# Kernel optimization log

Measured on AMD Instinct MI355X. Metric: run time of the kernel, lower is better.

Reference implementation:

```python
import jax, jax.numpy as jnp
import numpy as np

B, S, D, P = 8, 2048, 512, 64  # batch, seq, num_embed_hidden, num_attention_project


def setup_inputs() -> dict:
    key = jax.random.key(0)
    ks = jax.random.split(key, 9)
    sd = 1.0 / np.sqrt(D)
    sp = 1.0 / np.sqrt(P)
    return {
        "query": jax.random.normal(ks[0], (B, S, D), dtype=jnp.float32),
        "attention_mask": jnp.ones((B, S), dtype=jnp.float32),
        "Wq": jax.random.uniform(ks[1], (D, P), jnp.float32, -sd, sd),
        "bq": jax.random.uniform(ks[2], (P,), jnp.float32, -sd, sd),
        "Wk": jax.random.uniform(ks[3], (D, P), jnp.float32, -sd, sd),
        "bk": jax.random.uniform(ks[4], (P,), jnp.float32, -sd, sd),
        "Wv": jax.random.uniform(ks[5], (D, P), jnp.float32, -sd, sd),
        "bv": jax.random.uniform(ks[6], (P,), jnp.float32, -sd, sd),
        "Wo": jax.random.uniform(ks[7], (P, D), jnp.float32, -sp, sp),
        "bo": jax.random.uniform(ks[8], (D,), jnp.float32, -sp, sp),
    }


def reference(query, attention_mask, Wq, bq, Wk, bk, Wv, bv, Wo, bo):
    q = jnp.einsum("bsd,dp->bsp", query, Wq) + bq  # [B,S,P]
    k = jnp.einsum("bsd,dp->bsp", query, Wk) + bk
    v = jnp.einsum("bsd,dp->bsp", query, Wv) + bv
    scores = jnp.einsum("bsp,btp->bst", q, k) / jnp.sqrt(jnp.float32(P))  # [B,S,S]
    # Faithful to original: mask broadcast over last axis via unsqueeze(-1) -> masks rows
    scores = scores + (1.0 - attention_mask[:, :, None]) * -10000.0
    weights = jax.nn.softmax(scores, axis=-1)
    weighted = jnp.einsum("bst,btp->bsp", weights, v)
    return jnp.einsum("bsp,pd->bsd", weighted, Wo) + bo
```

## Files before the change

### kernel.cpp

```cpp
#include <hip/hip_runtime.h>
#include <hip/hip_bf16.h>
#include <math.h>

constexpr int B = 8;
constexpr int S = 2048;
constexpr int D = 512;
constexpr int P = 64;
constexpr float SCALE = 0.125f;

typedef short bf16x8 __attribute__((ext_vector_type(8)));
typedef float f32x4 __attribute__((ext_vector_type(4)));
typedef unsigned int u32;

__device__ __forceinline__ unsigned short f2bf(float x) {
  __hip_bfloat16 h = __float2bfloat16(x);
  return __builtin_bit_cast(unsigned short, h);
}
__device__ __forceinline__ float bf2f(unsigned short u) {
  unsigned int v = (unsigned int)u << 16;
  return __builtin_bit_cast(float, v);
}

__device__ __forceinline__ void ld_g2lds16(const unsigned short* g,
                                           unsigned short* l) {
  __builtin_amdgcn_global_load_lds(
      (const __attribute__((address_space(1))) u32*)g,
      (__attribute__((address_space(3))) u32*)l, 16, 0, 0);
}

__global__ __launch_bounds__(256) void prep_w(
    const float* __restrict__ Wq, const float* __restrict__ Wk,
    const float* __restrict__ Wv, const float* __restrict__ Wo,
    unsigned short* __restrict__ WcatT, unsigned short* __restrict__ WoT) {
  const int i = blockIdx.x * 256 + threadIdx.x;
  if (i < 192 * 512) {
    const int n = i >> 9, k = i & 511;
    const float* W = (n < 64) ? Wq : (n < 128) ? Wk : Wv;
    WcatT[i] = f2bf(W[k * 64 + (n & 63)]);
  }
  if (i < 512 * 64) {
    WoT[i] = f2bf(Wo[(i & 63) * 512 + (i >> 6)]);
  }
}

__global__ __launch_bounds__(256, 2) void qkv_mfma(
    const float* __restrict__ query, const unsigned short* __restrict__ WcatT,
    const float* __restrict__ bq, const float* __restrict__ bk,
    const float* __restrict__ bv, unsigned short* __restrict__ q_bf,
    unsigned short* __restrict__ k_bf, unsigned short* __restrict__ vT_bf) {
  __shared__ __align__(16) unsigned short Aq[32 * 512];
  __shared__ __align__(16) unsigned short Bb[2][192 * 64];

  const int tid = threadIdx.x;
  const int w = tid >> 6;
  const int l = tid & 63;
  const int l15 = l & 15;
  const int l4 = l >> 4;
  const int s0 = blockIdx.x * 32;
  const int rg = w & 1;
  const int ch = w >> 1;

  const float* qsrc = query + (size_t)s0 * D;
  for (int step = 0; step < 8; ++step) {
    const int row = step * 4 + w;
    const float* pf = qsrc + row * D + l * 8;
    const float4 x = *(const float4*)pf;
    const float4 y = *(const float4*)(pf + 4);
    bf16x8 u;
    u[0] = (short)f2bf(x.x); u[1] = (short)f2bf(x.y);
    u[2] = (short)f2bf(x.z); u[3] = (short)f2bf(x.w);
    u[4] = (short)f2bf(y.x); u[5] = (short)f2bf(y.y);
    u[6] = (short)f2bf(y.z); u[7] = (short)f2bf(y.w);
    *(bf16x8*)&Aq[row * 512 + ((l ^ (row & 7)) << 3)] = u;
  }

#pragma unroll
  for (int c = 0; c < 6; ++c) {
    const int n = c * 32 + w * 8 + (l >> 3);
    const unsigned short* gp =
        WcatT + (size_t)n * 512 + (((l & 7) ^ (l >> 3)) << 3);
    ld_g2lds16(gp, &Bb[0][(c * 256 + w * 64) * 8]);
  }
  __syncthreads();

  f32x4 acc[6];
#pragma unroll
  for (int nt = 0; nt < 6; ++nt) acc[nt] = (f32x4){0.f, 0.f, 0.f, 0.f};

  for (int kc = 0; kc < 8; ++kc) {
    if (kc < 7) {
#pragma unroll
      for (int c = 0; c < 6; ++c) {
        const int n = c * 32 + w * 8 + (l >> 3);
        const unsigned short* gp = WcatT + (size_t)n * 512 + (kc + 1) * 64 +
                                   (((l & 7) ^ (l >> 3)) << 3);
        ld_g2lds16(gp, &Bb[(kc + 1) & 1][(c * 256 + w * 64) * 8]);
      }
    }
    const unsigned short* Bcur = &Bb[kc & 1][0];
#pragma unroll
    for (int kk = 0; kk < 2; ++kk) {
      const int row = rg * 16 + l15;
      const int aslot = (kc * 8 + kk * 4 + l4) ^ (row & 7);
      const bf16x8 af = *(const bf16x8*)&Aq[row * 512 + (aslot << 3)];
      bf16x8 bfr[6];
#pragma unroll
      for (int nt = 0; nt < 6; ++nt) {
        const int n = ch * 96 + nt * 16 + l15;
        const int slot = (kk * 4 + l4) ^ (n & 7);
        bfr[nt] = *(const bf16x8*)&Bcur[n * 64 + (slot << 3)];
      }
#pragma unroll
      for (int nt = 0; nt < 6; ++nt)
        acc[nt] = __builtin_amdgcn_mfma_f32_16x16x32_bf16(af, bfr[nt], acc[nt],
                                                          0, 0, 0);
    }
    __syncthreads();
  }

  const int batch = s0 >> 11;
  const int sloc = s0 & 2047;
#pragma unroll
  for (int nt = 0; nt < 6; ++nt) {
    const int col = ch * 96 + nt * 16 + l15;
    const int mat = col >> 6;
    const int p = col & 63;
    const float bb = ((mat == 0) ? bq : (mat == 1) ? bk : bv)[p];
#pragma unroll
    for (int r = 0; r < 4; ++r) {
      const int row = rg * 16 + l4 * 4 + r;
      const float vl = acc[nt][r] + bb;
      if (mat == 0)
        q_bf[(size_t)(s0 + row) * P + p] = f2bf(vl * SCALE);
      else if (mat == 1)
        k_bf[(size_t)(s0 + row) * P + p] = f2bf(vl);
      else
        vT_bf[((size_t)batch * P + p) * S + sloc + row] = f2bf(vl);
    }
  }
}

__global__ __launch_bounds__(512, 2) void attn_fused(
    const unsigned short* __restrict__ q_bf,
    const unsigned short* __restrict__ k_bf,
    const unsigned short* __restrict__ vT_bf,
    const unsigned short* __restrict__ WoT, const float* __restrict__ bo,
    float* __restrict__ out) {
  __shared__ __align__(16) unsigned short kb[2][4][64 * 64];
  __shared__ __align__(16) unsigned short vb[2][4][64 * 64];
  __shared__ __align__(16) unsigned short e_s[8][16 * 64];
  __shared__ float l_s[8][32];

  const int tid = threadIdx.x;
  const int w = tid >> 6;
  const int lane = tid & 63;
  const int l15 = lane & 15;
  const int l4 = lane >> 4;
  const int qg = w & 1;
  const int th = w >> 1;

  const int blk = blockIdx.x;
  const int b = blk & 7;
  const int s0 = (blk >> 3) * 64;

  const unsigned short* qb = q_bf + ((size_t)b * S + s0) * P;
  const unsigned short* kbg = k_bf + (size_t)b * S * P;
  const unsigned short* vtg = vT_bf + (size_t)b * P * S;

  bf16x8 aq[2][2];
#pragma unroll
  for (int st = 0; st < 2; ++st)
#pragma unroll
    for (int h = 0; h < 2; ++h)
      aq[st][h] = *(const bf16x8*)(qb + (size_t)(qg * 32 + st * 16 + l15) * P +
                                   h * 32 + l4 * 8);

  f32x4 acc[2][4];
#pragma unroll
  for (int st = 0; st < 2; ++st)
#pragma unroll
    for (int pc = 0; pc < 4; ++pc) acc[st][pc] = (f32x4){0.f, 0.f, 0.f, 0.f};
  float lpart[2][4] = {{0.f, 0.f, 0.f, 0.f}, {0.f, 0.f, 0.f, 0.f}};

  const int jrow = (lane >> 3);
  const int jch = lane & 7;
  {
    const int t0 = th * 512;
#pragma unroll
    for (int j = 0; j < 8; ++j) {
      if (qg == 0) {
        const unsigned short* gp =
            kbg + ((size_t)t0 + j * 8 + jrow) * P + jch * 8;
        ld_g2lds16(gp, &kb[0][th][j * 512]);
      } else {
        const unsigned short* gp =
            vtg + ((size_t)(j * 8 + jrow)) * S + t0 + jch * 8;
        ld_g2lds16(gp, &vb[0][th][j * 512]);
      }
    }
  }
  __syncthreads();

  for (int win = 0; win < 8; ++win) {
    if (win < 7) {
      const int t0n = th * 512 + (win + 1) * 64;
      const int nb = (win + 1) & 1;
#pragma unroll
      for (int j = 0; j < 8; ++j) {
        if (qg == 0) {
          const unsigned short* gp =
              kbg + ((size_t)t0n + j * 8 + jrow) * P + jch * 8;
          ld_g2lds16(gp, &kb[nb][th][j * 512]);
        } else {
          const unsigned short* gp =
              vtg + ((size_t)(j * 8 + jrow)) * S + t0n + jch * 8;
          ld_g2lds16(gp, &vb[nb][th][j * 512]);
        }
      }
    }

    const unsigned short* kt = &kb[win & 1][th][0];
    const unsigned short* vt = &vb[win & 1][th][0];

    bf16x8 bkf[4][2], bvf[4][2];
#pragma unroll
    for (int nt = 0; nt < 4; ++nt)
#pragma unroll
      for (int h = 0; h < 2; ++h)
        bkf[nt][h] =
            *(const bf16x8*)&kt[(nt * 16 + l15) * 64 + h * 32 + l4 * 8];
#pragma unroll
    for (int pc = 0; pc < 4; ++pc)
#pragma unroll
      for (int kk = 0; kk < 2; ++kk)
        bvf[pc][kk] =
            *(const bf16x8*)&vt[(pc * 16 + l15) * 64 + kk * 32 + l4 * 8];

#pragma unroll
    for (int st = 0; st < 2; ++st) {
      f32x4 sc[4];
#pragma unroll
      for (int nt = 0; nt < 4; ++nt) {
        f32x4 c = (f32x4){0.f, 0.f, 0.f, 0.f};
        c = __builtin_amdgcn_mfma_f32_16x16x32_bf16(aq[st][0], bkf[nt][0], c,
                                                    0, 0, 0);
        sc[nt] = __builtin_amdgcn_mfma_f32_16x16x32_bf16(aq[st][1], bkf[nt][1],
                                                         c, 0, 0, 0);
      }
#pragma unroll
      for (int nt = 0; nt < 4; ++nt) {
        const int ch = nt * 2 + (l15 >> 3);
#pragma unroll
        for (int r = 0; r < 4; ++r) {
          const int rr = l4 * 4 + r;
          const unsigned short eu = f2bf(__expf(sc[nt][r]));
          lpart[st][r] += bf2f(eu);
          e_s[w][rr * 64 + ((ch ^ (rr & 7)) << 3) + (l15 & 7)] = eu;
        }
      }
      bf16x8 ae[2];
#pragma unroll
      for (int kk = 0; kk < 2; ++kk)
        ae[kk] = *(const bf16x8*)&e_s[w][l15 * 64 +
                                         (((kk * 4 + l4) ^ (l15 & 7)) << 3)];
#pragma unroll
      for (int pc = 0; pc < 4; ++pc) {
        acc[st][pc] = __builtin_amdgcn_mfma_f32_16x16x32_bf16(
            ae[0], bvf[pc][0], acc[st][pc], 0, 0, 0);
        acc[st][pc] = __builtin_amdgcn_mfma_f32_16x16x32_bf16(
            ae[1], bvf[pc][1], acc[st][pc], 0, 0, 0);
      }
    }
    __syncthreads();
  }

#pragma unroll
  for (int st = 0; st < 2; ++st) {
#pragma unroll
    for (int r = 0; r < 4; ++r) {
      float v = lpart[st][r];
      v += __shfl_xor(v, 1, 64);
      v += __shfl_xor(v, 2, 64);
      v += __shfl_xor(v, 4, 64);
      v += __shfl_xor(v, 8, 64);
      if (l15 == 0) l_s[w][st * 16 + l4 * 4 + r] = v;
    }
  }

  float* pacc = (float*)&kb[0][0][0];
  if (th > 0) {
#pragma unroll
    for (int st = 0; st < 2; ++st)
#pragma unroll
      for (int pc = 0; pc < 4; ++pc)
#pragma unroll
        for (int r = 0; r < 4; ++r)
          pacc[((size_t)(qg * 3 + th - 1) * 32 + st * 16 + l4 * 4 + r) * 64 +
               pc * 16 + l15] = acc[st][pc][r];
  }
  __syncthreads();

  unsigned short* wnorm = &e_s[0][0];
  if (th == 0) {
#pragma unroll
    for (int st = 0; st < 2; ++st) {
      float rl[4];
#pragma unroll
      for (int r = 0; r < 4; ++r) {
        const int row = st * 16 + l4 * 4 + r;
        rl[r] = 1.f / (l_s[qg][row] + l_s[2 + qg][row] + l_s[4 + qg][row] +
                       l_s[6 + qg][row]);
      }
#pragma unroll
      for (int pc = 0; pc < 4; ++pc)
#pragma unroll
        for (int r = 0; r < 4; ++r) {
          float s = acc[st][pc][r];
#pragma unroll
          for (int j = 0; j < 3; ++j)
            s += pacc[((size_t)(qg * 3 + j) * 32 + st * 16 + l4 * 4 + r) * 64 +
                      pc * 16 + l15];
          wnorm[(qg * 32 + st * 16 + l4 * 4 + r) * 64 + pc * 16 + l15] =
              f2bf(s * rl[r]);
        }
    }
  }
  __syncthreads();

  const int sub = w & 3;
  const int chalf = w >> 2;
  const int qgs = sub >> 1;
  const int lrow = (sub & 1) * 16 + l15;
  const bf16x8 a0 = *(const bf16x8*)&wnorm[(qgs * 32 + lrow) * 64 + l4 * 8];
  const bf16x8 a1 =
      *(const bf16x8*)&wnorm[(qgs * 32 + lrow) * 64 + 32 + l4 * 8];
  const size_t orow0 = (size_t)b * S + s0 + sub * 16;
#pragma unroll
  for (int ct = 0; ct < 16; ++ct) {
    const int col = chalf * 256 + ct * 16 + l15;
    const bf16x8 b0 = *(const bf16x8*)(WoT + (size_t)col * 64 + l4 * 8);
    const bf16x8 b1 = *(const bf16x8*)(WoT + (size_t)col * 64 + 32 + l4 * 8);
    f32x4 c = (f32x4){0.f, 0.f, 0.f, 0.f};
    c = __builtin_amdgcn_mfma_f32_16x16x32_bf16(a0, b0, c, 0, 0, 0);
    c = __builtin_amdgcn_mfma_f32_16x16x32_bf16(a1, b1, c, 0, 0, 0);
    const float bb = bo[col];
#pragma unroll
    for (int r = 0; r < 4; ++r)
      out[(orow0 + l4 * 4 + r) * D + col] = c[r] + bb;
  }
}

extern "C" void kernel_launch(void* const* d_in, const int* in_sizes, int n_in,
                              void* d_out, int out_size, void* d_ws,
                              size_t ws_size, hipStream_t stream) {
  const float* query = (const float*)d_in[0];
  const float* Wq = (const float*)d_in[2];
  const float* bq = (const float*)d_in[3];
  const float* Wk = (const float*)d_in[4];
  const float* bk = (const float*)d_in[5];
  const float* Wv = (const float*)d_in[6];
  const float* bv = (const float*)d_in[7];
  const float* Wo = (const float*)d_in[8];
  const float* bo = (const float*)d_in[9];
  float* out = (float*)d_out;

  const size_t n_rows = (size_t)B * S;
  const size_t proj = n_rows * P;
  unsigned short* qbf = (unsigned short*)d_ws;
  unsigned short* kbf = qbf + proj;
  unsigned short* vtbf = kbf + proj;
  unsigned short* WcatT = vtbf + proj;
  unsigned short* WoT = WcatT + 192 * 512;

  prep_w<<<384, 256, 0, stream>>>(Wq, Wk, Wv, Wo, WcatT, WoT);
  qkv_mfma<<<512, 256, 0, stream>>>(query, WcatT, bq, bk, bv, qbf, kbf, vtbf);
  attn_fused<<<256, 512, 0, stream>>>(qbf, kbf, vtbf, WoT, bo, out);
}
```

Baseline: 140.2 us.

## Store Q/K/V and weights in MFMA fragment layout, drop LDS staging

Intermediate Q, K, V and the weight matrices are now written in a pre-swizzled MFMA fragment order, so each lane loads its operand with one contiguous 16-byte global read. The async global-to-LDS double buffering and per-window block barriers in the attention kernel are removed, and the QKV kernel now uses 16-row tiles with more blocks and a higher occupancy hint. The aim is to cut LDS traffic and synchronisation, relying on L2 and cache for K/V reuse. The risk is that repeated global reads across waves lose the sharing the LDS staging gave and expose load latency without explicit prefetch.

```diff
diff --git a/kernel.cpp b/kernel.cpp
--- a/kernel.cpp
+++ b/kernel.cpp
@@ -21,47 +21,48 @@
   return __builtin_bit_cast(float, v);
 }
 
-__device__ __forceinline__ void ld_g2lds16(const unsigned short* g,
-                                           unsigned short* l) {
-  __builtin_amdgcn_global_load_lds(
-      (const __attribute__((address_space(1))) u32*)g,
-      (__attribute__((address_space(3))) u32*)l, 16, 0, 0);
-}
 
 __global__ __launch_bounds__(256) void prep_w(
     const float* __restrict__ Wq, const float* __restrict__ Wk,
     const float* __restrict__ Wv, const float* __restrict__ Wo,
-    unsigned short* __restrict__ WcatT, unsigned short* __restrict__ WoT) {
+    unsigned short* __restrict__ Bfrag, unsigned short* __restrict__ Wofrag) {
   const int i = blockIdx.x * 256 + threadIdx.x;
   if (i < 192 * 512) {
-    const int n = i >> 9, k = i & 511;
+    const int d = i / 192;
+    const int n = i - d * 192;
     const float* W = (n < 64) ? Wq : (n < 128) ? Wk : Wv;
-    WcatT[i] = f2bf(W[k * 64 + (n & 63)]);
-  }
-  if (i < 512 * 64) {
-    WoT[i] = f2bf(Wo[(i & 63) * 512 + (i >> 6)]);
-  }
-}
-
-__global__ __launch_bounds__(256, 2) void qkv_mfma(
-    const float* __restrict__ query, const unsigned short* __restrict__ WcatT,
+    const float val = W[d * 64 + (n & 63)];
+    const int nt = n >> 4, l15 = n & 15;
+    const int k16 = d >> 5, l4 = (d >> 3) & 3, j = d & 7;
+    Bfrag[(((nt * 16 + k16) * 4 + l4) * 16 + l15) * 8 + j] = f2bf(val);
+  }
+  if (i < 64 * 512) {
+    const int k = i >> 9;
+    const int n = i & 511;
+    const float val = Wo[k * 512 + n];
+    const int ct = n >> 4, l15 = n & 15;
+    const int h = k >> 5, l4 = (k >> 3) & 3, j = k & 7;
+    Wofrag[(((ct * 2 + h) * 4 + l4) * 16 + l15) * 8 + j] = f2bf(val);
+  }
+}
+
+__global__ __launch_bounds__(256, 4) void qkv_mfma(
+    const float* __restrict__ query, const unsigned short* __restrict__ Bfrag,
     const float* __restrict__ bq, const float* __restrict__ bk,
-    const float* __restrict__ bv, unsigned short* __restrict__ q_bf,
-    unsigned short* __restrict__ k_bf, unsigned short* __restrict__ vT_bf) {
-  __shared__ __align__(16) unsigned short Aq[32 * 512];
-  __shared__ __align__(16) unsigned short Bb[2][192 * 64];
+    const float* __restrict__ bv, unsigned short* __restrict__ qfrag,
+    unsigned short* __restrict__ kfrag, unsigned short* __restrict__ vfrag) {
+  __shared__ __align__(16) unsigned short Aq[16 * 512];
 
   const int tid = threadIdx.x;
   const int w = tid >> 6;
   const int l = tid & 63;
   const int l15 = l & 15;
   const int l4 = l >> 4;
-  const int s0 = blockIdx.x * 32;
-  const int rg = w & 1;
-  const int ch = w >> 1;
+  const int s0 = blockIdx.x * 16;
 
   const float* qsrc = query + (size_t)s0 * D;
-  for (int step = 0; step < 8; ++step) {
+#pragma unroll
+  for (int step = 0; step < 4; ++step) {
     const int row = step * 4 + w;
     const float* pf = qsrc + row * D + l * 8;
     const float4 x = *(const float4*)pf;
@@ -73,82 +74,62 @@
     u[6] = (short)f2bf(y.z); u[7] = (short)f2bf(y.w);
     *(bf16x8*)&Aq[row * 512 + ((l ^ (row & 7)) << 3)] = u;
   }
-
-#pragma unroll
-  for (int c = 0; c < 6; ++c) {
-    const int n = c * 32 + w * 8 + (l >> 3);
-    const unsigned short* gp =
-        WcatT + (size_t)n * 512 + (((l & 7) ^ (l >> 3)) << 3);
-    ld_g2lds16(gp, &Bb[0][(c * 256 + w * 64) * 8]);
-  }
   __syncthreads();
 
-  f32x4 acc[6];
-#pragma unroll
-  for (int nt = 0; nt < 6; ++nt) acc[nt] = (f32x4){0.f, 0.f, 0.f, 0.f};
-
-  for (int kc = 0; kc < 8; ++kc) {
-    if (kc < 7) {
-#pragma unroll
-      for (int c = 0; c < 6; ++c) {
-        const int n = c * 32 + w * 8 + (l >> 3);
-        const unsigned short* gp = WcatT + (size_t)n * 512 + (kc + 1) * 64 +
-                                   (((l & 7) ^ (l >> 3)) << 3);
-        ld_g2lds16(gp, &Bb[(kc + 1) & 1][(c * 256 + w * 64) * 8]);
-      }
-    }
-    const unsigned short* Bcur = &Bb[kc & 1][0];
-#pragma unroll
-    for (int kk = 0; kk < 2; ++kk) {
-      const int row = rg * 16 + l15;
-      const int aslot = (kc * 8 + kk * 4 + l4) ^ (row & 7);
-      const bf16x8 af = *(const bf16x8*)&Aq[row * 512 + (aslot << 3)];
-      bf16x8 bfr[6];
-#pragma unroll
-      for (int nt = 0; nt < 6; ++nt) {
-        const int n = ch * 96 + nt * 16 + l15;
-        const int slot = (kk * 4 + l4) ^ (n & 7);
-        bfr[nt] = *(const bf16x8*)&Bcur[n * 64 + (slot << 3)];
-      }
-#pragma unroll
-      for (int nt = 0; nt < 6; ++nt)
-        acc[nt] = __builtin_amdgcn_mfma_f32_16x16x32_bf16(af, bfr[nt], acc[nt],
-                                                          0, 0, 0);
-    }
-    __syncthreads();
-  }
-
-  const int batch = s0 >> 11;
-  const int sloc = s0 & 2047;
-#pragma unroll
-  for (int nt = 0; nt < 6; ++nt) {
-    const int col = ch * 96 + nt * 16 + l15;
+  f32x4 acc[3];
+#pragma unroll
+  for (int nt = 0; nt < 3; ++nt) acc[nt] = (f32x4){0.f, 0.f, 0.f, 0.f};
+
+#pragma unroll
+  for (int k16 = 0; k16 < 16; ++k16) {
+    const int aslot = (k16 * 4 + l4) ^ (l15 & 7);
+    const bf16x8 af = *(const bf16x8*)&Aq[l15 * 512 + (aslot << 3)];
+#pragma unroll
+    for (int nt = 0; nt < 3; ++nt) {
+      const int ntg = w * 3 + nt;
+      const bf16x8 bf =
+          *(const bf16x8*)(Bfrag + ((size_t)(ntg * 16 + k16) * 64 + l) * 8);
+      acc[nt] = __builtin_amdgcn_mfma_f32_16x16x32_bf16(af, bf, acc[nt], 0, 0,
+                                                        0);
+    }
+  }
+
+  const int b = s0 >> 11;
+  const size_t bbase = (size_t)b * (S * P);
+#pragma unroll
+  for (int nt = 0; nt < 3; ++nt) {
+    const int col = w * 48 + nt * 16 + l15;
     const int mat = col >> 6;
     const int p = col & 63;
     const float bb = ((mat == 0) ? bq : (mat == 1) ? bk : bv)[p];
 #pragma unroll
     for (int r = 0; r < 4; ++r) {
-      const int row = rg * 16 + l4 * 4 + r;
+      const int s = s0 + l4 * 4 + r;
+      const int t = s & 2047;
       const float vl = acc[nt][r] + bb;
-      if (mat == 0)
-        q_bf[(size_t)(s0 + row) * P + p] = f2bf(vl * SCALE);
-      else if (mat == 1)
-        k_bf[(size_t)(s0 + row) * P + p] = f2bf(vl);
-      else
-        vT_bf[((size_t)batch * P + p) * S + sloc + row] = f2bf(vl);
-    }
-  }
-}
-
-__global__ __launch_bounds__(512, 2) void attn_fused(
-    const unsigned short* __restrict__ q_bf,
-    const unsigned short* __restrict__ k_bf,
-    const unsigned short* __restrict__ vT_bf,
-    const unsigned short* __restrict__ WoT, const float* __restrict__ bo,
+      if (mat == 2) {
+        const int tb = t >> 5, chv = (t >> 3) & 3, jv = t & 7;
+        const int pcv = p >> 4, rowv = p & 15;
+        vfrag[bbase + (((size_t)(tb * 4 + pcv) * 4 + chv) * 16 + rowv) * 8 +
+              jv] = f2bf(vl);
+      } else {
+        const int tile = t >> 4, rowin = t & 15;
+        const int h = p >> 5, chp = (p >> 3) & 3, j = p & 7;
+        unsigned short* dst = (mat == 0) ? qfrag : kfrag;
+        dst[bbase + (((size_t)(tile * 2 + h) * 4 + chp) * 16 + rowin) * 8 +
+            j] = f2bf(mat == 0 ? vl * SCALE : vl);
+      }
+    }
+  }
+}
+
+__global__ __launch_bounds__(512, 4) void attn_fused(
+    const unsigned short* __restrict__ qfrag,
+    const unsigned short* __restrict__ kfrag,
+    const unsigned short* __restrict__ vfrag,
+    const unsigned short* __restrict__ Wofrag, const float* __restrict__ bo,
     float* __restrict__ out) {
-  __shared__ __align__(16) unsigned short kb[2][4][64 * 64];
-  __shared__ __align__(16) unsigned short vb[2][4][64 * 64];
-  __shared__ __align__(16) unsigned short e_s[8][16 * 64];
+  __shared__ __align__(16) unsigned char smem[57344];
   __shared__ float l_s[8][32];
 
   const int tid = threadIdx.x;
@@ -163,17 +144,23 @@
   const int b = blk & 7;
   const int s0 = (blk >> 3) * 64;
 
-  const unsigned short* qb = q_bf + ((size_t)b * S + s0) * P;
-  const unsigned short* kbg = k_bf + (size_t)b * S * P;
-  const unsigned short* vtg = vT_bf + (size_t)b * P * S;
+  const size_t bbase = (size_t)b * (S * P);
+  const unsigned short* qf = qfrag + bbase;
+  const unsigned short* kf = kfrag + bbase;
+  const unsigned short* vf = vfrag + bbase;
+
+  unsigned short* e_s = (unsigned short*)smem + w * 2048;
 
   bf16x8 aq[2][2];
 #pragma unroll
   for (int st = 0; st < 2; ++st)
 #pragma unroll
     for (int h = 0; h < 2; ++h)
-      aq[st][h] = *(const bf16x8*)(qb + (size_t)(qg * 32 + st * 16 + l15) * P +
-                                   h * 32 + l4 * 8);
+      aq[st][h] = *(const bf16x8*)(qf +
+                                   ((size_t)(((s0 >> 4) + qg * 2 + st) * 2 + h) *
+                                        64 +
+                                    lane) *
+                                       8);
 
   f32x4 acc[2][4];
 #pragma unroll
@@ -182,100 +169,74 @@
     for (int pc = 0; pc < 4; ++pc) acc[st][pc] = (f32x4){0.f, 0.f, 0.f, 0.f};
   float lpart[2][4] = {{0.f, 0.f, 0.f, 0.f}, {0.f, 0.f, 0.f, 0.f}};
 
-  const int jrow = (lane >> 3);
-  const int jch = lane & 7;
-  {
-    const int t0 = th * 512;
-#pragma unroll
-    for (int j = 0; j < 8; ++j) {
-      if (qg == 0) {
-        const unsigned short* gp =
-            kbg + ((size_t)t0 + j * 8 + jrow) * P + jch * 8;
-        ld_g2lds16(gp, &kb[0][th][j * 512]);
-      } else {
-        const unsigned short* gp =
-            vtg + ((size_t)(j * 8 + jrow)) * S + t0 + jch * 8;
-        ld_g2lds16(gp, &vb[0][th][j * 512]);
-      }
-    }
-  }
-  __syncthreads();
-
   for (int win = 0; win < 8; ++win) {
-    if (win < 7) {
-      const int t0n = th * 512 + (win + 1) * 64;
-      const int nb = (win + 1) & 1;
-#pragma unroll
-      for (int j = 0; j < 8; ++j) {
-        if (qg == 0) {
-          const unsigned short* gp =
-              kbg + ((size_t)t0n + j * 8 + jrow) * P + jch * 8;
-          ld_g2lds16(gp, &kb[nb][th][j * 512]);
-        } else {
-          const unsigned short* gp =
-              vtg + ((size_t)(j * 8 + jrow)) * S + t0n + jch * 8;
-          ld_g2lds16(gp, &vb[nb][th][j * 512]);
-        }
-      }
-    }
-
-    const unsigned short* kt = &kb[win & 1][th][0];
-    const unsigned short* vt = &vb[win & 1][th][0];
-
-    bf16x8 bkf[4][2], bvf[4][2];
+    const int t0 = th * 512 + win * 64;
+
+    bf16x8 bk[4][2];
 #pragma unroll
     for (int nt = 0; nt < 4; ++nt)
 #pragma unroll
       for (int h = 0; h < 2; ++h)
-        bkf[nt][h] =
-            *(const bf16x8*)&kt[(nt * 16 + l15) * 64 + h * 32 + l4 * 8];
-#pragma unroll
-    for (int pc = 0; pc < 4; ++pc)
-#pragma unroll
-      for (int kk = 0; kk < 2; ++kk)
-        bvf[pc][kk] =
-            *(const bf16x8*)&vt[(pc * 16 + l15) * 64 + kk * 32 + l4 * 8];
-
-#pragma unroll
-    for (int st = 0; st < 2; ++st) {
-      f32x4 sc[4];
+        bk[nt][h] =
+            *(const bf16x8*)(kf +
+                             ((size_t)(((t0 >> 4) + nt) * 2 + h) * 64 + lane) *
+                                 8);
+
+    f32x4 sc[2][4];
+#pragma unroll
+    for (int st = 0; st < 2; ++st)
 #pragma unroll
       for (int nt = 0; nt < 4; ++nt) {
         f32x4 c = (f32x4){0.f, 0.f, 0.f, 0.f};
-        c = __builtin_amdgcn_mfma_f32_16x16x32_bf16(aq[st][0], bkf[nt][0], c,
-                                                    0, 0, 0);
-        sc[nt] = __builtin_amdgcn_mfma_f32_16x16x32_bf16(aq[st][1], bkf[nt][1],
-                                                         c, 0, 0, 0);
-      }
+        c = __builtin_amdgcn_mfma_f32_16x16x32_bf16(aq[st][0], bk[nt][0], c, 0,
+                                                    0, 0);
+        sc[st][nt] = __builtin_amdgcn_mfma_f32_16x16x32_bf16(
+            aq[st][1], bk[nt][1], c, 0, 0, 0);
+      }
+
+    bf16x8 bv[4][2];
+#pragma unroll
+    for (int pc = 0; pc < 4; ++pc)
+#pragma unroll
+      for (int kk = 0; kk < 2; ++kk)
+        bv[pc][kk] =
+            *(const bf16x8*)(vf +
+                             ((size_t)(((t0 >> 5) + kk) * 4 + pc) * 64 + lane) *
+                                 8);
+
+#pragma unroll
+    for (int st = 0; st < 2; ++st)
 #pragma unroll
       for (int nt = 0; nt < 4; ++nt) {
         const int ch = nt * 2 + (l15 >> 3);
 #pragma unroll
         for (int r = 0; r < 4; ++r) {
           const int rr = l4 * 4 + r;
-          const unsigned short eu = f2bf(__expf(sc[nt][r]));
+          const unsigned short eu = f2bf(__expf(sc[st][nt][r]));
           lpart[st][r] += bf2f(eu);
-          e_s[w][rr * 64 + ((ch ^ (rr & 7)) << 3) + (l15 & 7)] = eu;
+          e_s[st * 1024 + rr * 64 + ((ch ^ (rr & 7)) << 3) + (l15 & 7)] = eu;
         }
       }
+
+#pragma unroll
+    for (int st = 0; st < 2; ++st) {
       bf16x8 ae[2];
 #pragma unroll
       for (int kk = 0; kk < 2; ++kk)
-        ae[kk] = *(const bf16x8*)&e_s[w][l15 * 64 +
-                                         (((kk * 4 + l4) ^ (l15 & 7)) << 3)];
+        ae[kk] = *(const bf16x8*)&e_s[st * 1024 + l15 * 64 +
+                                      (((kk * 4 + l4) ^ (l15 & 7)) << 3)];
 #pragma unroll
       for (int pc = 0; pc < 4; ++pc) {
         acc[st][pc] = __builtin_amdgcn_mfma_f32_16x16x32_bf16(
-            ae[0], bvf[pc][0], acc[st][pc], 0, 0, 0);
+            ae[0], bv[pc][0], acc[st][pc], 0, 0, 0);
         acc[st][pc] = __builtin_amdgcn_mfma_f32_16x16x32_bf16(
-            ae[1], bvf[pc][1], acc[st][pc], 0, 0, 0);
-      }
-    }
-    __syncthreads();
-  }
-
-#pragma unroll
-  for (int st = 0; st < 2; ++st) {
+            ae[1], bv[pc][1], acc[st][pc], 0, 0, 0);
+      }
+    }
+  }
+
+#pragma unroll
+  for (int st = 0; st < 2; ++st)
 #pragma unroll
     for (int r = 0; r < 4; ++r) {
       float v = lpart[st][r];
@@ -285,9 +246,10 @@
       v += __shfl_xor(v, 8, 64);
       if (l15 == 0) l_s[w][st * 16 + l4 * 4 + r] = v;
     }
-  }
-
-  float* pacc = (float*)&kb[0][0][0];
+
+  __syncthreads();
+
+  float* pacc = (float*)smem;
   if (th > 0) {
 #pragma unroll
     for (int st = 0; st < 2; ++st)
@@ -300,7 +262,7 @@
   }
   __syncthreads();
 
-  unsigned short* wnorm = &e_s[0][0];
+  unsigned short* wnorm = (unsigned short*)(smem + 49152);
   if (th == 0) {
 #pragma unroll
     for (int st = 0; st < 2; ++st) {
@@ -329,20 +291,21 @@
 
   const int sub = w & 3;
   const int chalf = w >> 2;
-  const int qgs = sub >> 1;
-  const int lrow = (sub & 1) * 16 + l15;
-  const bf16x8 a0 = *(const bf16x8*)&wnorm[(qgs * 32 + lrow) * 64 + l4 * 8];
+  const bf16x8 a0 = *(const bf16x8*)&wnorm[(sub * 16 + l15) * 64 + l4 * 8];
   const bf16x8 a1 =
-      *(const bf16x8*)&wnorm[(qgs * 32 + lrow) * 64 + 32 + l4 * 8];
+      *(const bf16x8*)&wnorm[(sub * 16 + l15) * 64 + 32 + l4 * 8];
   const size_t orow0 = (size_t)b * S + s0 + sub * 16;
 #pragma unroll
   for (int ct = 0; ct < 16; ++ct) {
-    const int col = chalf * 256 + ct * 16 + l15;
-    const bf16x8 b0 = *(const bf16x8*)(WoT + (size_t)col * 64 + l4 * 8);
-    const bf16x8 b1 = *(const bf16x8*)(WoT + (size_t)col * 64 + 32 + l4 * 8);
+    const int ctg = chalf * 16 + ct;
+    const bf16x8 b0 =
+        *(const bf16x8*)(Wofrag + ((size_t)(ctg * 2 + 0) * 64 + lane) * 8);
+    const bf16x8 b1 =
+        *(const bf16x8*)(Wofrag + ((size_t)(ctg * 2 + 1) * 64 + lane) * 8);
     f32x4 c = (f32x4){0.f, 0.f, 0.f, 0.f};
     c = __builtin_amdgcn_mfma_f32_16x16x32_bf16(a0, b0, c, 0, 0, 0);
     c = __builtin_amdgcn_mfma_f32_16x16x32_bf16(a1, b1, c, 0, 0, 0);
+    const int col = ctg * 16 + l15;
     const float bb = bo[col];
 #pragma unroll
     for (int r = 0; r < 4; ++r)
@@ -364,15 +327,14 @@
   const float* bo = (const float*)d_in[9];
   float* out = (float*)d_out;
 
-  const size_t n_rows = (size_t)B * S;
-  const size_t proj = n_rows * P;
-  unsigned short* qbf = (unsigned short*)d_ws;
-  unsigned short* kbf = qbf + proj;
-  unsigned short* vtbf = kbf + proj;
-  unsigned short* WcatT = vtbf + proj;
-  unsigned short* WoT = WcatT + 192 * 512;
-
-  prep_w<<<384, 256, 0, stream>>>(Wq, Wk, Wv, Wo, WcatT, WoT);
-  qkv_mfma<<<512, 256, 0, stream>>>(query, WcatT, bq, bk, bv, qbf, kbf, vtbf);
-  attn_fused<<<256, 512, 0, stream>>>(qbf, kbf, vtbf, WoT, bo, out);
-}
+  const size_t proj = (size_t)B * S * P;
+  unsigned short* qfr = (unsigned short*)d_ws;
+  unsigned short* kfr = qfr + proj;
+  unsigned short* vfr = kfr + proj;
+  unsigned short* Bfrag = vfr + proj;
+  unsigned short* Wofrag = Bfrag + 192 * 512;
+
+  prep_w<<<384, 256, 0, stream>>>(Wq, Wk, Wv, Wo, Bfrag, Wofrag);
+  qkv_mfma<<<1024, 256, 0, stream>>>(query, Bfrag, bq, bk, bv, qfr, kfr, vfr);
+  attn_fused<<<256, 512, 0, stream>>>(qfr, kfr, vfr, Wofrag, bo, out);
+}
```

New measurement: 142.4 us. About the same (+1.6%).
